# Performance work log

Hardware: AMD Instinct MI355X
Metric: run time of the kernel (lower is better)

Reference implementation:

```python
import jax, jax.numpy as jnp
import numpy as np

NX, NY, NZ = 432, 496, 1
C = 64  # num_bev_features


def setup_inputs() -> dict:
    key = jax.random.key(0)
    k1, k2, k3, k4 = jax.random.split(key, 4)
    P = 128000
    B = 8
    pillar_features = jax.random.normal(k1, (P, C), dtype=jnp.float32)
    coords_b = jax.random.randint(k2, (P,), 0, B, dtype=jnp.int32)
    coords_z = jnp.zeros((P,), dtype=jnp.int32)
    coords_y = jax.random.randint(k3, (P,), 0, NY, dtype=jnp.int32)
    coords_x = jax.random.randint(k4, (P,), 0, NX, dtype=jnp.int32)
    return {
        "pillar_features": pillar_features,
        "coords_b": coords_b,
        "coords_z": coords_z,
        "coords_y": coords_y,
        "coords_x": coords_x,
        "batch_size": 8,
    }


def reference(pillar_features, coords_b, coords_z, coords_y, coords_x, batch_size):
    # flat spatial index exactly as the torch code: z + y*nx + x  (nz == 1 -> z == 0)
    idx = (coords_z + coords_y * NX + coords_x).astype(jnp.int32)  # [P]
    # one fused scatter over all batches: out[b, :, idx] = pillar_features[p, :]
    out = jnp.zeros((batch_size, C, NZ * NY * NX), dtype=pillar_features.dtype)
    out = out.at[coords_b, :, idx].set(pillar_features)
    return out.reshape(batch_size, C * NZ, NY, NX)
```

## Files before the change

kernel.cpp:

```cpp
#include <hip/hip_runtime.h>


#define NXx 432
#define NYy 496
#define SS  (NXx * NYy)
#define CC  64
#define TS  2048
#define CG  8

typedef float f4 __attribute__((ext_vector_type(4)));

__global__ void winner_kernel(const int* __restrict__ cb,
                              const int* __restrict__ cz,
                              const int* __restrict__ cy,
                              const int* __restrict__ cx,
                              int* __restrict__ winner, int P) {
    int p = blockIdx.x * blockDim.x + threadIdx.x;
    if (p < P) {
        int slot = cb[p] * SS + cz[p] + cy[p] * NXx + cx[p];
        atomicMax(&winner[slot], p);
    }
}

__global__ __launch_bounds__(256)
void scatter_kernel(const float* __restrict__ pf,
                    const int* __restrict__ winner,
                    float* __restrict__ out) {
    __shared__ float lds[CG][TS];
    const int t    = threadIdx.x;
    const int wave = t >> 6;
    const int lane = t & 63;
    const int slot0 = blockIdx.x * TS;

    int w[8];
    #pragma unroll
    for (int k = 0; k < 8; ++k) w[k] = winner[slot0 + k * 256 + t];

    for (int cg = 0; cg < CC / CG; ++cg) {
        #pragma unroll
        for (int k = 0; k < 8; ++k) {
            const int sl = k * 256 + t;
            float v[CG];
            if (w[k] >= 0) {
                const f4* row = reinterpret_cast<const f4*>(
                    pf + (size_t)w[k] * CC + cg * CG);
                f4 a = row[0], bq = row[1];
                v[0]=a.x;  v[1]=a.y;  v[2]=a.z;  v[3]=a.w;
                v[4]=bq.x; v[5]=bq.y; v[6]=bq.z; v[7]=bq.w;
            } else {
                #pragma unroll
                for (int c = 0; c < CG; ++c) v[c] = 0.0f;
            }
            #pragma unroll
            for (int c = 0; c < CG; ++c)
                lds[c][sl] = v[c];
        }
        __syncthreads();

        #pragma unroll
        for (int pl = 0; pl < 2; ++pl) {
            const int c = wave * 2 + pl;
            const int gc = cg * CG + c;
            #pragma unroll
            for (int i = 0; i < 8; ++i) {
                const int off = i * 256 + 4 * lane;
                f4 v = *reinterpret_cast<const f4*>(&lds[c][off]);
                const int gs = slot0 + off;
                const int b  = gs / SS;
                const int s  = gs - b * SS;
                *reinterpret_cast<f4*>(out + (size_t)(b * CC + gc) * SS + s) = v;
            }
        }
        __syncthreads();
    }
}

extern "C" void kernel_launch(void* const* d_in, const int* in_sizes, int n_in,
                              void* d_out, int out_size, void* d_ws, size_t ws_size,
                              hipStream_t stream) {
    const float* pf = (const float*)d_in[0];
    const int* cb   = (const int*)d_in[1];
    const int* cz   = (const int*)d_in[2];
    const int* cy   = (const int*)d_in[3];
    const int* cx   = (const int*)d_in[4];
    float* out      = (float*)d_out;

    const int P      = in_sizes[1];
    const int nslots = out_size / CC;

    int* winner = (int*)d_ws;
    hipMemsetAsync(winner, 0xFF, (size_t)nslots * sizeof(int), stream);

    winner_kernel<<<(P + 255) / 256, 256, 0, stream>>>(cb, cz, cy, cx, winner, P);

    scatter_kernel<<<nslots / TS, 256, 0, stream>>>(pf, winner, out);
}
```

Baseline: 500.9 us.

## Make scatter transpose wave-private to replace block barriers with wave barriers

Each wave now owns a 256-slot tile with its own LDS region, so the transpose needs only wave-level barriers instead of block-wide __syncthreads. The block tile shrinks from 2048 to 1024 slots, which increases the grid size and lowers LDS use per block. The launch-bounds hint requests more resident blocks. Each wave now writes 1 KB contiguous runs per channel, shorter than the 8 KB runs per channel before. The batch index is computed once per wave rather than per store.

```diff
diff --git a/kernel.cpp b/kernel.cpp
--- a/kernel.cpp
+++ b/kernel.cpp
@@ -5,7 +5,7 @@
 #define NYy 496
 #define SS  (NXx * NYy)
 #define CC  64
-#define TS  2048
+#define TSW 256
 #define CG  8
 
 typedef float f4 __attribute__((ext_vector_type(4)));
@@ -22,24 +22,30 @@
     }
 }
 
-__global__ __launch_bounds__(256)
+__global__ __launch_bounds__(256, 5)
 void scatter_kernel(const float* __restrict__ pf,
                     const int* __restrict__ winner,
                     float* __restrict__ out) {
-    __shared__ float lds[CG][TS];
+    __shared__ float lds[4][CG][TSW];
     const int t    = threadIdx.x;
     const int wave = t >> 6;
     const int lane = t & 63;
-    const int slot0 = blockIdx.x * TS;
 
-    int w[8];
+    const int sbase = blockIdx.x * (4 * TSW) + wave * TSW;
+    const int b  = sbase / SS;
+    const int s0 = sbase - b * SS;
+    float* const obase = out + (size_t)(b * CC) * SS + s0 + 4 * lane;
+
+    int w[4];
     #pragma unroll
-    for (int k = 0; k < 8; ++k) w[k] = winner[slot0 + k * 256 + t];
+    for (int k = 0; k < 4; ++k) w[k] = winner[sbase + k * 64 + lane];
+
+    float (*L)[TSW] = lds[wave];
 
     for (int cg = 0; cg < CC / CG; ++cg) {
         #pragma unroll
-        for (int k = 0; k < 8; ++k) {
-            const int sl = k * 256 + t;
+        for (int k = 0; k < 4; ++k) {
+            const int sl = k * 64 + lane;
             float v[CG];
             if (w[k] >= 0) {
                 const f4* row = reinterpret_cast<const f4*>(
@@ -53,25 +59,16 @@
             }
             #pragma unroll
             for (int c = 0; c < CG; ++c)
-                lds[c][sl] = v[c];
+                L[c][sl] = v[c];
         }
-        __syncthreads();
+        __builtin_amdgcn_wave_barrier();
 
         #pragma unroll
-        for (int pl = 0; pl < 2; ++pl) {
-            const int c = wave * 2 + pl;
-            const int gc = cg * CG + c;
-            #pragma unroll
-            for (int i = 0; i < 8; ++i) {
-                const int off = i * 256 + 4 * lane;
-                f4 v = *reinterpret_cast<const f4*>(&lds[c][off]);
-                const int gs = slot0 + off;
-                const int b  = gs / SS;
-                const int s  = gs - b * SS;
-                *reinterpret_cast<f4*>(out + (size_t)(b * CC + gc) * SS + s) = v;
-            }
+        for (int c = 0; c < CG; ++c) {
+            f4 v = *reinterpret_cast<const f4*>(&L[c][4 * lane]);
+            *reinterpret_cast<f4*>(obase + (size_t)(cg * CG + c) * SS) = v;
         }
-        __syncthreads();
+        __builtin_amdgcn_wave_barrier();
     }
 }
 
@@ -93,5 +90,5 @@
 
     winner_kernel<<<(P + 255) / 256, 256, 0, stream>>>(cb, cz, cy, cx, winner, P);
 
-    scatter_kernel<<<nslots / TS, 256, 0, stream>>>(pf, winner, out);
+    scatter_kernel<<<nslots / (4 * TSW), 256, 0, stream>>>(pf, winner, out);
 }
```

New measurement: 484.7 us. 3.2% less time.
